# Kernel tuning notes

Hardware: AMD Instinct MI355X
Metric: run time of the kernel (lower is better)

## Reference

```python
import jax, jax.numpy as jnp
import numpy as np

LORA_SCALING = 1.0 / 2.0  # lora_alpha / lora_r = 1/2


def _qlora_linear(x, wq, A, B):
    # wq: (out, in/4) fake-NF4 compressed weight, repeated x4 -> (out, in)
    w = jnp.tile(wq, (1, 4))
    base = x @ w.T                              # (..., out)
    lora = (x @ A.T) @ B.T                      # low-rank path, r=2
    return base + lora * LORA_SCALING


def setup_inputs() -> dict:
    key = jax.random.key(0)
    ks = jax.random.split(key, 10)
    d, h, r = 4096, 11008, 2
    return {
        "x":   jax.random.normal(ks[0], (16, 1, d), dtype=jnp.float32),
        "w1q": jax.random.normal(ks[1], (h, d // 4), dtype=jnp.float32) * 0.02,
        "a1":  jax.random.normal(ks[2], (r, d), dtype=jnp.float32) * 0.02,
        "b1":  jax.random.normal(ks[3], (h, r), dtype=jnp.float32) * 0.02,
        "w3q": jax.random.normal(ks[4], (h, d // 4), dtype=jnp.float32) * 0.02,
        "a3":  jax.random.normal(ks[5], (r, d), dtype=jnp.float32) * 0.02,
        "b3":  jax.random.normal(ks[6], (h, r), dtype=jnp.float32) * 0.02,
        "w2q": jax.random.normal(ks[7], (d, h // 4), dtype=jnp.float32) * 0.02,
        "a2":  jax.random.normal(ks[8], (r, h), dtype=jnp.float32) * 0.02,
        "b2":  jax.random.normal(ks[9], (d, r), dtype=jnp.float32) * 0.02,
    }


def reference(x, w1q, a1, b1, w3q, a3, b3, w2q, a2, b2):
    # SwiGLU MLP: w2( silu(w1(x)) * w3(x) ), each linear = repeat-dequant + LoRA
    gate = jax.nn.silu(_qlora_linear(x, w1q, a1, b1))  # (B, S, hidden)
    up = _qlora_linear(x, w3q, a3, b3)                 # (B, S, hidden)
    return _qlora_linear(gate * up, w2q, a2, b2)       # (B, S, d_model)
```

## Files before the change

### kernel.cpp

```cpp
#include <hip/hip_runtime.h>
#include <hip/hip_bf16.h>


#define NB     16
#define DMODEL 4096
#define HID    11008
#define DQ     1024
#define HQ     2752

#define XSB_OFF 0
#define T1_OFF  8192
#define T3_OFF  8224
#define HVT_OFF 8256
#define HSB_OFF 184384
#define T2_OFF  206400

typedef __attribute__((ext_vector_type(8))) short bf16x8;
typedef __attribute__((ext_vector_type(4))) float f32x4;

__device__ __forceinline__ unsigned short f2bf(float f) {
  unsigned u = __float_as_uint(f);
  unsigned r = u + 0x7fffu + ((u >> 16) & 1u);
  return (unsigned short)(r >> 16);
}
__device__ __forceinline__ unsigned pack2(float lo, float hi) {
  return (unsigned)f2bf(lo) | ((unsigned)f2bf(hi) << 16);
}
__device__ __forceinline__ bf16x8 cvt8(const float4 a, const float4 b) {
  uint4 u = make_uint4(pack2(a.x, a.y), pack2(a.z, a.w),
                       pack2(b.x, b.y), pack2(b.z, b.w));
  return __builtin_bit_cast(bf16x8, u);
}

__global__ __launch_bounds__(256) void k_prep1(const float* __restrict__ x,
                                               const float* __restrict__ a1,
                                               const float* __restrict__ a3,
                                               float* __restrict__ ws) {
  const int b = blockIdx.x, t = threadIdx.x;
  const float4* x4  = (const float4*)(x) + b * (DMODEL / 4);
  const float4* a14 = (const float4*)a1;
  const float4* a34 = (const float4*)a3;
  float4 xs = make_float4(0.f, 0.f, 0.f, 0.f);
  float s10 = 0.f, s11 = 0.f, s30 = 0.f, s31 = 0.f;
#pragma unroll
  for (int k = 0; k < 4; ++k) {
    float4 xv  = x4[k * 256 + t];
    xs.x += xv.x; xs.y += xv.y; xs.z += xv.z; xs.w += xv.w;
    float4 a10 = a14[k * 256 + t];
    float4 a11 = a14[1024 + k * 256 + t];
    float4 a30 = a34[k * 256 + t];
    float4 a31 = a34[1024 + k * 256 + t];
    s10 += xv.x * a10.x + xv.y * a10.y + xv.z * a10.z + xv.w * a10.w;
    s11 += xv.x * a11.x + xv.y * a11.y + xv.z * a11.z + xv.w * a11.w;
    s30 += xv.x * a30.x + xv.y * a30.y + xv.z * a30.z + xv.w * a30.w;
    s31 += xv.x * a31.x + xv.y * a31.y + xv.z * a31.z + xv.w * a31.w;
  }
  ((uint2*)(ws + XSB_OFF))[b * 256 + t] =
      make_uint2(pack2(xs.x, xs.y), pack2(xs.z, xs.w));

  __shared__ float4 rb[256];
  rb[t] = make_float4(s10, s11, s30, s31);
  __syncthreads();
  for (int s = 128; s > 0; s >>= 1) {
    if (t < s) {
      rb[t].x += rb[t + s].x; rb[t].y += rb[t + s].y;
      rb[t].z += rb[t + s].z; rb[t].w += rb[t + s].w;
    }
    __syncthreads();
  }
  if (t == 0) {
    ws[T1_OFF + b * 2]     = rb[0].x;
    ws[T1_OFF + b * 2 + 1] = rb[0].y;
    ws[T3_OFF + b * 2]     = rb[0].z;
    ws[T3_OFF + b * 2 + 1] = rb[0].w;
  }
}

__global__ __launch_bounds__(256) void k_gateup(const float* __restrict__ w1q,
                                                const float* __restrict__ w3q,
                                                const float* __restrict__ b1,
                                                const float* __restrict__ b3,
                                                const float* __restrict__ ws,
                                                float* __restrict__ hvecT) {
  __shared__ float red[4][8][64];
  const int t = threadIdx.x, w = t >> 6, l = t & 63;
  const int tile = blockIdx.x;
  const int n  = l & 15;
  const int kb = (l >> 4) * 8;
  const int o  = tile * 16 + n;
  const unsigned short* xsb = (const unsigned short*)(ws + XSB_OFF);

  f32x4 acc1 = {0.f, 0.f, 0.f, 0.f}, acc3 = {0.f, 0.f, 0.f, 0.f};
  const int k0 = w * 256;
#pragma unroll
  for (int kk = 0; kk < 8; ++kk) {
    const int kabs = k0 + kk * 32 + kb;
    const float4* p1 = (const float4*)(w1q + (size_t)o * DQ + kabs);
    const float4* p3 = (const float4*)(w3q + (size_t)o * DQ + kabs);
    const bf16x8 bb = *(const bf16x8*)(xsb + n * DQ + kabs);
    const bf16x8 a1f = cvt8(p1[0], p1[1]);
    const bf16x8 a3f = cvt8(p3[0], p3[1]);
    acc1 = __builtin_amdgcn_mfma_f32_16x16x32_bf16(a1f, bb, acc1, 0, 0, 0);
    acc3 = __builtin_amdgcn_mfma_f32_16x16x32_bf16(a3f, bb, acc3, 0, 0, 0);
  }
#pragma unroll
  for (int r = 0; r < 4; ++r) {
    red[w][r][l]     = acc1[r];
    red[w][r + 4][l] = acc3[r];
  }
  __syncthreads();
  if (w == 0) {
    const float t10 = ws[T1_OFF + 2 * n], t11 = ws[T1_OFF + 2 * n + 1];
    const float t30 = ws[T3_OFF + 2 * n], t31 = ws[T3_OFF + 2 * n + 1];
    const int m4 = (l >> 4) * 4;
#pragma unroll
    for (int r = 0; r < 4; ++r) {
      const float g0 = red[0][r][l] + red[1][r][l] + red[2][r][l] + red[3][r][l];
      const float u0 = red[0][r + 4][l] + red[1][r + 4][l] +
                       red[2][r + 4][l] + red[3][r + 4][l];
      const int oo = tile * 16 + m4 + r;
      const float g = g0 + 0.5f * (t10 * b1[2 * oo] + t11 * b1[2 * oo + 1]);
      const float u = u0 + 0.5f * (t30 * b3[2 * oo] + t31 * b3[2 * oo + 1]);
      hvecT[oo * 16 + n] = (g / (1.f + __expf(-g))) * u;
    }
  }
}

__global__ __launch_bounds__(256) void k_prep2(const float* __restrict__ hvecT,
                                               const float* __restrict__ a2,
                                               float* __restrict__ ws) {
  const int b = blockIdx.x, t = threadIdx.x;
  float s0 = 0.f, s1 = 0.f;
  unsigned short* hsb = (unsigned short*)(ws + HSB_OFF);
  for (int j = t; j < HQ; j += 256) {
    float v0 = hvecT[j * 16 + b];
    float v1 = hvecT[(j + HQ) * 16 + b];
    float v2 = hvecT[(j + 2 * HQ) * 16 + b];
    float v3 = hvecT[(j + 3 * HQ) * 16 + b];
    hsb[b * HQ + j] = f2bf(v0 + v1 + v2 + v3);
    s0 += v0 * a2[j] + v1 * a2[j + HQ] + v2 * a2[j + 2 * HQ] + v3 * a2[j + 3 * HQ];
    s1 += v0 * a2[HID + j] + v1 * a2[HID + j + HQ] +
          v2 * a2[HID + j + 2 * HQ] + v3 * a2[HID + j + 3 * HQ];
  }
  __shared__ float2 rb[256];
  rb[t] = make_float2(s0, s1);
  __syncthreads();
  for (int s = 128; s > 0; s >>= 1) {
    if (t < s) { rb[t].x += rb[t + s].x; rb[t].y += rb[t + s].y; }
    __syncthreads();
  }
  if (t == 0) { ws[T2_OFF + b * 2] = rb[0].x; ws[T2_OFF + b * 2 + 1] = rb[0].y; }
}

__global__ __launch_bounds__(256) void k_down(const float* __restrict__ w2q,
                                              const float* __restrict__ b2,
                                              const float* __restrict__ ws,
                                              float* __restrict__ out) {
  __shared__ float red[4][4][64];
  const int t = threadIdx.x, w = t >> 6, l = t & 63;
  const int tile = blockIdx.x;
  const int n  = l & 15;
  const int kb = (l >> 4) * 8;
  const int o  = tile * 16 + n;
  const unsigned short* hsb = (const unsigned short*)(ws + HSB_OFF);

  f32x4 acc = {0.f, 0.f, 0.f, 0.f};
  const int kks  = (w < 2) ? w * 22 : 44 + (w - 2) * 21;
  const int klen = (w < 2) ? 22 : 21;
#pragma unroll
  for (int kk = 0; kk < 22; ++kk) {
    if (kk < klen) {
      const int kabs = (kks + kk) * 32 + kb;
      const float4* p2 = (const float4*)(w2q + (size_t)o * HQ + kabs);
      const bf16x8 bb = *(const bf16x8*)(hsb + n * HQ + kabs);
      const bf16x8 af = cvt8(p2[0], p2[1]);
      acc = __builtin_amdgcn_mfma_f32_16x16x32_bf16(af, bb, acc, 0, 0, 0);
    }
  }
#pragma unroll
  for (int r = 0; r < 4; ++r) red[w][r][l] = acc[r];
  __syncthreads();
  if (w == 0) {
    const float t20 = ws[T2_OFF + 2 * n], t21 = ws[T2_OFF + 2 * n + 1];
    const int m4 = (l >> 4) * 4;
#pragma unroll
    for (int r = 0; r < 4; ++r) {
      const float v = red[0][r][l] + red[1][r][l] + red[2][r][l] + red[3][r][l];
      const int oo = tile * 16 + m4 + r;
      out[n * DMODEL + oo] = v + 0.5f * (t20 * b2[2 * oo] + t21 * b2[2 * oo + 1]);
    }
  }
}

extern "C" void kernel_launch(void* const* d_in, const int* in_sizes, int n_in,
                              void* d_out, int out_size, void* d_ws, size_t ws_size,
                              hipStream_t stream) {
  const float* x   = (const float*)d_in[0];
  const float* w1q = (const float*)d_in[1];
  const float* a1  = (const float*)d_in[2];
  const float* b1  = (const float*)d_in[3];
  const float* w3q = (const float*)d_in[4];
  const float* a3  = (const float*)d_in[5];
  const float* b3  = (const float*)d_in[6];
  const float* w2q = (const float*)d_in[7];
  const float* a2  = (const float*)d_in[8];
  const float* b2  = (const float*)d_in[9];
  float* out = (float*)d_out;
  float* ws  = (float*)d_ws;
  float* hvecT = ws + HVT_OFF;

  k_prep1<<<16, 256, 0, stream>>>(x, a1, a3, ws);
  k_gateup<<<HID / 16, 256, 0, stream>>>(w1q, w3q, b1, b3, ws, hvecT);
  k_prep2<<<16, 256, 0, stream>>>(hvecT, a2, ws);
  k_down<<<DMODEL / 16, 256, 0, stream>>>(w2q, b2, ws, out);
}
```

Baseline: 48.87 us.

## Widen gate/up and down blocks to 8 waves and parallelize prep2 with atomics

Gate/up and down GEMV kernels now use 512-thread blocks, so each of 8 waves handles half as much of the K split. Partials are reduced across 8 waves in shared memory. prep2 is restructured from 16 blocks looping over the hidden dim to 172 blocks, each covering 16 columns. Within a block it reduces with shuffles and accumulates the LoRA dot products via atomicAdd into a buffer that prep1 zeroes. The bf16 conversion also switches to the HIP intrinsic. This targets low parallelism and latency in the small kernels, at the cost of atomic ordering nondeterminism and larger blocks.

After: 49.96 us. +2.2%, slower.

```diff
diff --git a/kernel.cpp b/kernel.cpp
--- a/kernel.cpp
+++ b/kernel.cpp
@@ -18,13 +18,12 @@
 typedef __attribute__((ext_vector_type(8))) short bf16x8;
 typedef __attribute__((ext_vector_type(4))) float f32x4;
 
-__device__ __forceinline__ unsigned short f2bf(float f) {
-  unsigned u = __float_as_uint(f);
-  unsigned r = u + 0x7fffu + ((u >> 16) & 1u);
-  return (unsigned short)(r >> 16);
+__device__ __forceinline__ unsigned short f2bfh(float f) {
+  __hip_bfloat16 h = __float2bfloat16(f);
+  return __builtin_bit_cast(unsigned short, h);
 }
 __device__ __forceinline__ unsigned pack2(float lo, float hi) {
-  return (unsigned)f2bf(lo) | ((unsigned)f2bf(hi) << 16);
+  return (unsigned)f2bfh(lo) | ((unsigned)f2bfh(hi) << 16);
 }
 __device__ __forceinline__ bf16x8 cvt8(const float4 a, const float4 b) {
   uint4 u = make_uint4(pack2(a.x, a.y), pack2(a.z, a.w),
@@ -37,6 +36,8 @@
                                                const float* __restrict__ a3,
                                                float* __restrict__ ws) {
   const int b = blockIdx.x, t = threadIdx.x;
+  if (b == 0 && t < 32) ws[T2_OFF + t] = 0.f;
+
   const float4* x4  = (const float4*)(x) + b * (DMODEL / 4);
   const float4* a14 = (const float4*)a1;
   const float4* a34 = (const float4*)a3;
@@ -76,13 +77,13 @@
   }
 }
 
-__global__ __launch_bounds__(256) void k_gateup(const float* __restrict__ w1q,
+__global__ __launch_bounds__(512) void k_gateup(const float* __restrict__ w1q,
                                                 const float* __restrict__ w3q,
                                                 const float* __restrict__ b1,
                                                 const float* __restrict__ b3,
                                                 const float* __restrict__ ws,
                                                 float* __restrict__ hvecT) {
-  __shared__ float red[4][8][64];
+  __shared__ float red[8][8][64];
   const int t = threadIdx.x, w = t >> 6, l = t & 63;
   const int tile = blockIdx.x;
   const int n  = l & 15;
@@ -91,9 +92,9 @@
   const unsigned short* xsb = (const unsigned short*)(ws + XSB_OFF);
 
   f32x4 acc1 = {0.f, 0.f, 0.f, 0.f}, acc3 = {0.f, 0.f, 0.f, 0.f};
-  const int k0 = w * 256;
-#pragma unroll
-  for (int kk = 0; kk < 8; ++kk) {
+  const int k0 = w * 128;
+#pragma unroll
+  for (int kk = 0; kk < 4; ++kk) {
     const int kabs = k0 + kk * 32 + kb;
     const float4* p1 = (const float4*)(w1q + (size_t)o * DQ + kabs);
     const float4* p3 = (const float4*)(w3q + (size_t)o * DQ + kabs);
@@ -115,9 +116,12 @@
     const int m4 = (l >> 4) * 4;
 #pragma unroll
     for (int r = 0; r < 4; ++r) {
-      const float g0 = red[0][r][l] + red[1][r][l] + red[2][r][l] + red[3][r][l];
-      const float u0 = red[0][r + 4][l] + red[1][r + 4][l] +
-                       red[2][r + 4][l] + red[3][r + 4][l];
+      float g0 = 0.f, u0 = 0.f;
+#pragma unroll
+      for (int ww = 0; ww < 8; ++ww) {
+        g0 += red[ww][r][l];
+        u0 += red[ww][r + 4][l];
+      }
       const int oo = tile * 16 + m4 + r;
       const float g = g0 + 0.5f * (t10 * b1[2 * oo] + t11 * b1[2 * oo + 1]);
       const float u = u0 + 0.5f * (t30 * b3[2 * oo] + t31 * b3[2 * oo + 1]);
@@ -129,34 +133,37 @@
 __global__ __launch_bounds__(256) void k_prep2(const float* __restrict__ hvecT,
                                                const float* __restrict__ a2,
                                                float* __restrict__ ws) {
-  const int b = blockIdx.x, t = threadIdx.x;
-  float s0 = 0.f, s1 = 0.f;
+  const int t = threadIdx.x;
+  const int b = t >> 4, jl = t & 15;
+  const int j = blockIdx.x * 16 + jl;
   unsigned short* hsb = (unsigned short*)(ws + HSB_OFF);
-  for (int j = t; j < HQ; j += 256) {
-    float v0 = hvecT[j * 16 + b];
-    float v1 = hvecT[(j + HQ) * 16 + b];
-    float v2 = hvecT[(j + 2 * HQ) * 16 + b];
-    float v3 = hvecT[(j + 3 * HQ) * 16 + b];
-    hsb[b * HQ + j] = f2bf(v0 + v1 + v2 + v3);
-    s0 += v0 * a2[j] + v1 * a2[j + HQ] + v2 * a2[j + 2 * HQ] + v3 * a2[j + 3 * HQ];
-    s1 += v0 * a2[HID + j] + v1 * a2[HID + j + HQ] +
-          v2 * a2[HID + j + 2 * HQ] + v3 * a2[HID + j + 3 * HQ];
-  }
-  __shared__ float2 rb[256];
-  rb[t] = make_float2(s0, s1);
-  __syncthreads();
-  for (int s = 128; s > 0; s >>= 1) {
-    if (t < s) { rb[t].x += rb[t + s].x; rb[t].y += rb[t + s].y; }
-    __syncthreads();
-  }
-  if (t == 0) { ws[T2_OFF + b * 2] = rb[0].x; ws[T2_OFF + b * 2 + 1] = rb[0].y; }
-}
-
-__global__ __launch_bounds__(256) void k_down(const float* __restrict__ w2q,
+
+  const float v0 = hvecT[(size_t)j * 16 + b];
+  const float v1 = hvecT[(size_t)(j + HQ) * 16 + b];
+  const float v2 = hvecT[(size_t)(j + 2 * HQ) * 16 + b];
+  const float v3 = hvecT[(size_t)(j + 3 * HQ) * 16 + b];
+  hsb[b * HQ + j] = f2bfh(v0 + v1 + v2 + v3);
+
+  float s0 = v0 * a2[j] + v1 * a2[j + HQ] +
+             v2 * a2[j + 2 * HQ] + v3 * a2[j + 3 * HQ];
+  float s1 = v0 * a2[HID + j] + v1 * a2[HID + j + HQ] +
+             v2 * a2[HID + j + 2 * HQ] + v3 * a2[HID + j + 3 * HQ];
+#pragma unroll
+  for (int off = 1; off < 16; off <<= 1) {
+    s0 += __shfl_xor(s0, off);
+    s1 += __shfl_xor(s1, off);
+  }
+  if (jl == 0) {
+    atomicAdd(&ws[T2_OFF + 2 * b], s0);
+    atomicAdd(&ws[T2_OFF + 2 * b + 1], s1);
+  }
+}
+
+__global__ __launch_bounds__(512) void k_down(const float* __restrict__ w2q,
                                               const float* __restrict__ b2,
                                               const float* __restrict__ ws,
                                               float* __restrict__ out) {
-  __shared__ float red[4][4][64];
+  __shared__ float red[8][4][64];
   const int t = threadIdx.x, w = t >> 6, l = t & 63;
   const int tile = blockIdx.x;
   const int n  = l & 15;
@@ -165,10 +172,10 @@
   const unsigned short* hsb = (const unsigned short*)(ws + HSB_OFF);
 
   f32x4 acc = {0.f, 0.f, 0.f, 0.f};
-  const int kks  = (w < 2) ? w * 22 : 44 + (w - 2) * 21;
-  const int klen = (w < 2) ? 22 : 21;
-#pragma unroll
-  for (int kk = 0; kk < 22; ++kk) {
+  const int kks  = (w < 6) ? w * 11 : 66 + (w - 6) * 10;
+  const int klen = (w < 6) ? 11 : 10;
+#pragma unroll
+  for (int kk = 0; kk < 11; ++kk) {
     if (kk < klen) {
       const int kabs = (kks + kk) * 32 + kb;
       const float4* p2 = (const float4*)(w2q + (size_t)o * HQ + kabs);
@@ -185,7 +192,9 @@
     const int m4 = (l >> 4) * 4;
 #pragma unroll
     for (int r = 0; r < 4; ++r) {
-      const float v = red[0][r][l] + red[1][r][l] + red[2][r][l] + red[3][r][l];
+      float v = 0.f;
+#pragma unroll
+      for (int ww = 0; ww < 8; ++ww) v += red[ww][r][l];
       const int oo = tile * 16 + m4 + r;
       out[n * DMODEL + oo] = v + 0.5f * (t20 * b2[2 * oo] + t21 * b2[2 * oo + 1]);
     }
@@ -210,7 +219,7 @@
   float* hvecT = ws + HVT_OFF;
 
   k_prep1<<<16, 256, 0, stream>>>(x, a1, a3, ws);
-  k_gateup<<<HID / 16, 256, 0, stream>>>(w1q, w3q, b1, b3, ws, hvecT);
-  k_prep2<<<16, 256, 0, stream>>>(hvecT, a2, ws);
-  k_down<<<DMODEL / 16, 256, 0, stream>>>(w2q, b2, ws, out);
-}
+  k_gateup<<<HID / 16, 512, 0, stream>>>(w1q, w3q, b1, b3, ws, hvecT);
+  k_prep2<<<HQ / 16, 256, 0, stream>>>(hvecT, a2, ws);
+  k_down<<<DMODEL / 16, 512, 0, stream>>>(w2q, b2, ws, out);
+}
```
